# Performance work log

Measured on AMD Instinct MI355X. Metric: run time of the kernel, lower is better.

The kernel has to match this reference:

```python
import jax, jax.numpy as jnp
import numpy as np

# Module config (matches init_kwargs): inp_modes=[16,4,4,4], out_modes=[16,4,4,4], ranks=[1,8,8,1], 3x3 kernel
C_IN0, C_OUT0 = 16, 16          # leading conv channels
INP_MODES = (4, 4, 4)            # TT input modes -> c_inp = 64
OUT_MODES = (4, 4, 4)            # TT output modes -> c_out = 64
RANKS = (1, 8, 8, 1)
C_INP = int(np.prod(INP_MODES))  # 64
C_OUT = int(np.prod(OUT_MODES))  # 64


def setup_inputs() -> dict:
    key = jax.random.key(0)
    ks = jax.random.split(key, 5)
    x = jax.random.normal(ks[0], (8, C_IN0 * C_INP, 64, 64), jnp.float32)
    kernel = jax.random.normal(ks[1], (C_OUT0, C_IN0, 3, 3), jnp.float32) * (2.0 / (C_IN0 + C_OUT0))
    cores = {}
    for k in range(3):
        m, n = INP_MODES[k], OUT_MODES[k]
        cores[f"core{k}"] = jax.random.normal(ks[2 + k], (RANKS[k], m, n, RANKS[k + 1]), jnp.float32) * (2.0 / (m + n))
    b = jnp.ones((C_OUT,), jnp.float32)
    return {"x": x, "kernel": kernel, **cores, "b": b}


def _tt_matrix(core0, core1, core2):
    # Reconstruct W[(i1 i2 i3), (j1 j2 j3)] from TT cores (r_k, m_k, n_k, r_{k+1}).
    Wm = core0[0]  # (m1, n1, r1)  since r0 == 1
    for c in (core1, core2):
        Wm = jnp.einsum('...r,rmns->...mns', Wm, c)  # append (m_k, n_k) modes
    Wm = Wm[..., 0]  # drop trailing rank (== 1): (m1,n1,m2,n2,m3,n3)
    Wm = jnp.transpose(Wm, (0, 2, 4, 1, 3, 5))       # (m1,m2,m3,n1,n2,n3)
    return Wm.reshape(C_INP, C_OUT)


def reference(x, kernel, core0, core1, core2, b):
    B, Cin, H, W = x.shape  # Cin = C_IN0 * C_INP
    xr = x.reshape(-1, C_IN0, H, W)  # (B*c_inp, c_inp_0, H, W)
    y = jax.lax.conv_general_dilated(
        xr, kernel, window_strides=(1, 1), padding='VALID',
        dimension_numbers=('NCHW', 'OIHW', 'NCHW'))  # (B*c_inp, c_out_0, h, w)
    h, w = y.shape[-2], y.shape[-1]
    # Follow the torch reshape chain exactly
    y = y.reshape(B, C_INP, -1)                 # (B, c_inp, c_out_0*h*w)
    y = jnp.transpose(y, (0, 2, 1)).reshape(-1, C_INP)  # (B*c_out_0*h*w, c_inp)
    Wm = _tt_matrix(core0, core1, core2)        # (c_inp, c_out)
    out = y @ Wm + b                             # (B*c_out_0*h*w, c_out)
    return out.reshape(B, C_OUT0 * C_OUT, h, w)
```

## Files before the change

kernel.cpp:

```cpp
#include <hip/hip_runtime.h>
#include <hip/hip_bf16.h>

#define NB    8
#define NG    64
#define NCI   16
#define NC0   16
#define NJ    64
#define IH    64
#define IW    64
#define OH    62
#define OW    62
#define IPIX  4096
#define OPIX  3844

typedef __attribute__((ext_vector_type(8))) short  short8;
typedef __attribute__((ext_vector_type(4))) short  short4v;
typedef __attribute__((ext_vector_type(4))) float  float4v;

__device__ __forceinline__ unsigned short f2bf(float f) {
    unsigned int u = __builtin_bit_cast(unsigned int, f);
    unsigned int r = (u + 0x7fffu + ((u >> 16) & 1u)) >> 16;
    return (unsigned short)r;
}

__global__ __launch_bounds__(64) void prep_kernel(const float* __restrict__ K,
                                                  const float* __restrict__ c0_,
                                                  const float* __restrict__ c1_,
                                                  const float* __restrict__ c2_,
                                                  unsigned short* __restrict__ wmb,
                                                  unsigned short* __restrict__ kb) {
    int bi = blockIdx.x;
    int l  = threadIdx.x;
    if (bi < 8) {
        int jt = bi >> 1, kh = bi & 1;
        int j = jt * 16 + (l & 15);
        int j1 = j >> 4, j2 = (j >> 2) & 3, j3 = j & 3;
        for (int i = 0; i < 8; ++i) {
            int g = kh * 32 + (l >> 4) * 8 + i;
            int i1 = g >> 4, i2 = (g >> 2) & 3, i3 = g & 3;
            float s = 0.f;
            #pragma unroll
            for (int r1 = 0; r1 < 8; ++r1) {
                float a = c0_[(i1 * 4 + j1) * 8 + r1];
                float t = 0.f;
                #pragma unroll
                for (int r2 = 0; r2 < 8; ++r2) {
                    t += c1_[((r1 * 4 + i2) * 4 + j2) * 8 + r2] *
                         c2_[(r2 * 4 + i3) * 4 + j3];
                }
                s += a * t;
            }
            wmb[(bi * 64 + l) * 8 + i] = f2bf(s);
        }
    } else {
        int c0i = l & 15, q = l >> 4;
        for (int f = 0; f < 5; ++f) {
            int tap = f * 2 + (q >> 1);
            for (int i = 0; i < 8; ++i) {
                int ci = (q & 1) * 8 + i;
                float v = (tap < 9) ? K[(c0i * 16 + ci) * 9 + tap] : 0.f;
                kb[(f * 64 + l) * 8 + i] = f2bf(v);
            }
        }
    }
}

__global__ __launch_bounds__(256) void conv1_kernel(const float* __restrict__ x,
                                                    const unsigned short* __restrict__ kb,
                                                    unsigned short* __restrict__ y) {
    __shared__ unsigned short xl[18 * 16 * 68];
    int t    = threadIdx.x;
    int bi   = blockIdx.x;
    int band = bi & 3;
    int g    = (bi >> 2) & 63;
    int b    = bi >> 8;
    int y0   = band * 16;

    {
        int ci = t >> 4, part = t & 15;
        const float* xc = x + ((size_t)(b * 1024 + g * 16 + ci) * IPIX);
        #pragma unroll
        for (int s = 0; s < 18; ++s) {
            int row = y0 + s; if (row > 63) row = 63;
            float4v v = *(const float4v*)(xc + row * 64 + part * 4);
            unsigned short* dst = xl + (s * 16 + ci) * 68 + part * 4;
            dst[0] = f2bf(v[0]); dst[1] = f2bf(v[1]);
            dst[2] = f2bf(v[2]); dst[3] = f2bf(v[3]);
        }
    }
    for (int e = t; e < 576; e += 256) {
        int r = e >> 5, rem = e & 31;
        xl[(r * 16 + (rem >> 1)) * 68 + 64 + (rem & 1)] = 0;
    }
    __syncthreads();

    int lane = t & 63, wv = t >> 6;
    int ln = lane & 15, quad = lane >> 4;

    short8 kf[5];
    #pragma unroll
    for (int f = 0; f < 5; ++f)
        kf[f] = *(const short8*)(kb + (f * 64 + lane) * 8);

    int ci0 = (quad & 1) * 8;
    for (int k = 0; k < 16; ++k) {
        int tid = wv * 16 + k;
        int yr = tid >> 2, xt = tid & 3, x0 = xt * 16;
        int yo = y0 + yr;
        float4v acc = {0.f, 0.f, 0.f, 0.f};
        #pragma unroll
        for (int f = 0; f < 5; ++f) {
            int tap = f * 2 + (quad >> 1);
            if (tap > 8) tap = 8;
            int dy = tap / 3, dx = tap % 3;
            const unsigned short* base = xl + ((yr + dy) * 16 + ci0) * 68 + x0 + dx + ln;
            short8 a;
            #pragma unroll
            for (int i = 0; i < 8; ++i) a[i] = (short)base[i * 68];
            acc = __builtin_amdgcn_mfma_f32_16x16x32_bf16(a, kf[f], acc, 0, 0, 0);
        }
        if (yo < OH) {
            unsigned short* yp = y + ((size_t)(b * 1024 + g * 16 + ln) * 4096
                                      + yo * 64 + x0 + quad * 4);
            short4v o;
            o[0] = (short)f2bf(acc[0]); o[1] = (short)f2bf(acc[1]);
            o[2] = (short)f2bf(acc[2]); o[3] = (short)f2bf(acc[3]);
            *(short4v*)yp = o;
        }
    }
}

__global__ __launch_bounds__(512, 2) void mix3_kernel(const unsigned short* __restrict__ y,
                                                      const unsigned short* __restrict__ wmb,
                                                      const float* __restrict__ bias,
                                                      float* __restrict__ out) {
    __shared__ __align__(16) unsigned short yl[64 * 1024];
    int t    = threadIdx.x;
    int bi   = blockIdx.x;
    int prow = bi % OH;
    int b    = bi / OH;

    {
        int pq = t & 7, grp = t >> 3;
        const unsigned short* yb = y + ((size_t)b * 1024 * 4096) + prow * 64 + pq * 8;
        #pragma unroll
        for (int it = 0; it < 4; ++it) {
            int qd = it * 64 + grp;
            int gq = qd & 15, c0 = qd >> 4;
            const unsigned short* yp = yb + (size_t)(gq * 4 * 16 + c0) * 4096;
            short8 v0 = *(const short8*)(yp);
            short8 v1 = *(const short8*)(yp + 16 * 4096);
            short8 v2 = *(const short8*)(yp + 32 * 4096);
            short8 v3 = *(const short8*)(yp + 48 * 4096);
            int chunk = gq >> 1;
            int gof   = (gq & 1) * 4;
            #pragma unroll
            for (int pp = 0; pp < 8; ++pp) {
                int px = pq * 8 + pp;
                int csw = chunk ^ (c0 & 7) ^ (pq & 7);
                short4v u;
                u[0] = v0[pp]; u[1] = v1[pp]; u[2] = v2[pp]; u[3] = v3[pp];
                *(short4v*)(yl + px * 1024 + c0 * 64 + csw * 8 + gof) = u;
            }
        }
    }
    __syncthreads();

    int lane = t & 63, wv = t >> 6;
    int ln = lane & 15, quad = lane >> 4;

    short8 bf[8];
    #pragma unroll
    for (int q8 = 0; q8 < 8; ++q8)
        bf[q8] = *(const short8*)(wmb + (q8 * 64 + lane) * 8);

    float4v bv[4];
    #pragma unroll
    for (int jt = 0; jt < 4; ++jt)
        bv[jt] = *(const float4v*)(bias + jt * 16 + quad * 4);

    for (int kk = 0; kk < 8; ++kk) {
        int pl = wv * 8 + kk;
        const unsigned short* arow = yl + pl * 1024 + ln * 64;
        int sx = (ln & 7) ^ ((pl >> 3) & 7);
        short8 a0 = *(const short8*)(arow + (((0 + quad) ^ sx) * 8));
        short8 a1 = *(const short8*)(arow + (((4 + quad) ^ sx) * 8));
        if (pl < OW) {
            float* ob = out + (((size_t)(b * 16 + ln) * OPIX) + prow * OW + pl) * NJ
                        + quad * 4;
            #pragma unroll
            for (int jt = 0; jt < 4; ++jt) {
                float4v acc = bv[jt];
                acc = __builtin_amdgcn_mfma_f32_16x16x32_bf16(bf[jt * 2 + 0], a0, acc, 0, 0, 0);
                acc = __builtin_amdgcn_mfma_f32_16x16x32_bf16(bf[jt * 2 + 1], a1, acc, 0, 0, 0);
                *(float4v*)(ob + jt * 16) = acc;
            }
        }
    }
}

__global__ __launch_bounds__(64) void wm_kernel(const float* __restrict__ core0,
                                                const float* __restrict__ core1,
                                                const float* __restrict__ core2,
                                                float* __restrict__ Wm) {
    int g = threadIdx.x;
    int i1 = g >> 4, i2 = (g >> 2) & 3, i3 = g & 3;
    for (int j = 0; j < NJ; ++j) {
        int j1 = j >> 4, j2 = (j >> 2) & 3, j3 = j & 3;
        float s = 0.f;
        #pragma unroll
        for (int r1 = 0; r1 < 8; ++r1) {
            float a = core0[(i1 * 4 + j1) * 8 + r1];
            float t = 0.f;
            #pragma unroll
            for (int r2 = 0; r2 < 8; ++r2) {
                t += core1[((r1 * 4 + i2) * 4 + j2) * 8 + r2] *
                     core2[(r2 * 4 + i3) * 4 + j3];
            }
            s += a * t;
        }
        Wm[g * NJ + j] = s;
    }
}

__global__ __launch_bounds__(256) void fused_fallback(const float* __restrict__ x,
                                                      const float* __restrict__ K,
                                                      const float* __restrict__ Wm,
                                                      const float* __restrict__ bias,
                                                      float* __restrict__ out) {
    __shared__ float wlds[NG * NJ];
    __shared__ float klds[NCI * 9];
    int blk  = blockIdx.x;
    int pblk = blk & 15;
    int c0   = (blk >> 4) & 15;
    int b    = blk >> 8;
    for (int i = threadIdx.x; i < NG * NJ; i += 256) wlds[i] = Wm[i];
    for (int i = threadIdx.x; i < NCI * 9; i += 256) klds[i] = K[c0 * NCI * 9 + i];
    __syncthreads();

    int pix = pblk * 256 + threadIdx.x;
    if (pix >= OPIX) return;
    int yy = pix / OW;
    int xx = pix % OW;

    float acc[NJ];
    #pragma unroll
    for (int j = 0; j < NJ; ++j) acc[j] = 0.f;

    for (int g = 0; g < NG; ++g) {
        float c = 0.f;
        const float* xb = x + ((size_t)(b * NG + g) * NCI) * IPIX;
        for (int ci = 0; ci < NCI; ++ci) {
            #pragma unroll
            for (int dy = 0; dy < 3; ++dy) {
                #pragma unroll
                for (int dx = 0; dx < 3; ++dx) {
                    c += xb[ci * IPIX + (yy + dy) * IW + (xx + dx)] *
                         klds[ci * 9 + dy * 3 + dx];
                }
            }
        }
        const float4* wp = (const float4*)&wlds[g * NJ];
        #pragma unroll
        for (int j4 = 0; j4 < 16; ++j4) {
            float4 w = wp[j4];
            acc[j4 * 4 + 0] += w.x * c;
            acc[j4 * 4 + 1] += w.y * c;
            acc[j4 * 4 + 2] += w.z * c;
            acc[j4 * 4 + 3] += w.w * c;
        }
    }
    #pragma unroll
    for (int j = 0; j < NJ; ++j) {
        out[(((size_t)(b * NC0 + c0) * OPIX) + pix) * NJ + j] = acc[j] + bias[j];
    }
}

extern "C" void kernel_launch(void* const* d_in, const int* in_sizes, int n_in,
                              void* d_out, int out_size, void* d_ws, size_t ws_size,
                              hipStream_t stream) {
    const float* x     = (const float*)d_in[0];
    const float* K     = (const float*)d_in[1];
    const float* core0 = (const float*)d_in[2];
    const float* core1 = (const float*)d_in[3];
    const float* core2 = (const float*)d_in[4];
    const float* bias  = (const float*)d_in[5];
    float* out = (float*)d_out;

    const size_t z_off   = 16384;
    const size_t z_bytes = (size_t)NB * 1024 * 4096 * sizeof(unsigned short);

    if (ws_size >= z_off + z_bytes + 256) {
        unsigned short* wmb = (unsigned short*)d_ws;
        unsigned short* kb  = (unsigned short*)((char*)d_ws + 8192);
        unsigned short* y   = (unsigned short*)((char*)d_ws + z_off);
        prep_kernel<<<9, 64, 0, stream>>>(K, core0, core1, core2, wmb, kb);
        conv1_kernel<<<NB * NG * 4, 256, 0, stream>>>(x, kb, y);
        mix3_kernel<<<NB * OH, 512, 0, stream>>>(y, wmb, bias, out);
    } else {
        float* Wm = (float*)d_ws;
        wm_kernel<<<1, 64, 0, stream>>>(core0, core1, core2, Wm);
        fused_fallback<<<NB * NC0 * 16, 256, 0, stream>>>(x, K, Wm, bias, out);
    }
}
```

Before: 99.55 us.

## Store conv input tile channel-innermost in LDS for vectorized MFMA operand loads

Changes the shared-memory tile layout in conv1 from [row][ci][x] to [row][x][ci] with a padded pixel stride of 20. Each lane can then fetch its 8 channel values for an MFMA A-operand with two 8-byte LDS reads instead of eight scalar 2-byte reads. The global-to-LDS staging is reorganized so each thread loads four channels and writes packed short4 vectors. Per-tap offsets are also hoisted out of the inner loop. The risks are LDS bank conflicts from the new stride and a different global load pattern.

```diff
diff --git a/kernel.cpp b/kernel.cpp
--- a/kernel.cpp
+++ b/kernel.cpp
@@ -65,10 +65,13 @@
     }
 }
 
+#define PXS  20
+#define ROWS 1320
+
 __global__ __launch_bounds__(256) void conv1_kernel(const float* __restrict__ x,
                                                     const unsigned short* __restrict__ kb,
                                                     unsigned short* __restrict__ y) {
-    __shared__ unsigned short xl[18 * 16 * 68];
+    __shared__ unsigned short xl[18 * ROWS];
     int t    = threadIdx.x;
     int bi   = blockIdx.x;
     int band = bi & 3;
@@ -77,20 +80,32 @@
     int y0   = band * 16;
 
     {
-        int ci = t >> 4, part = t & 15;
-        const float* xc = x + ((size_t)(b * 1024 + g * 16 + ci) * IPIX);
-        #pragma unroll
-        for (int s = 0; s < 18; ++s) {
-            int row = y0 + s; if (row > 63) row = 63;
-            float4v v = *(const float4v*)(xc + row * 64 + part * 4);
-            unsigned short* dst = xl + (s * 16 + ci) * 68 + part * 4;
-            dst[0] = f2bf(v[0]); dst[1] = f2bf(v[1]);
-            dst[2] = f2bf(v[2]); dst[3] = f2bf(v[3]);
-        }
-    }
-    for (int e = t; e < 576; e += 256) {
-        int r = e >> 5, rem = e & 31;
-        xl[(r * 16 + (rem >> 1)) * 68 + 64 + (rem & 1)] = 0;
+        int part = t & 15, cig = (t >> 4) & 3, sg = t >> 6;
+        const float* xc = x + ((size_t)(b * 1024 + g * 16 + cig * 4) * IPIX) + part * 4;
+        #pragma unroll
+        for (int k = 0; k < 5; ++k) {
+            int s = sg + k * 4;
+            if (s < 18) {
+                int row = y0 + s; if (row > 63) row = 63;
+                const float* xr = xc + row * 64;
+                float4v v0 = *(const float4v*)(xr);
+                float4v v1 = *(const float4v*)(xr + IPIX);
+                float4v v2 = *(const float4v*)(xr + 2 * IPIX);
+                float4v v3 = *(const float4v*)(xr + 3 * IPIX);
+                unsigned short* dst = xl + s * ROWS + (part * 4) * PXS + cig * 4;
+                #pragma unroll
+                for (int p = 0; p < 4; ++p) {
+                    short4v u;
+                    u[0] = (short)f2bf(v0[p]); u[1] = (short)f2bf(v1[p]);
+                    u[2] = (short)f2bf(v2[p]); u[3] = (short)f2bf(v3[p]);
+                    *(short4v*)(dst + p * PXS) = u;
+                }
+            }
+        }
+    }
+    for (int e = t; e < 18 * 32; e += 256) {
+        int s = e >> 5, rem = e & 31;
+        xl[s * ROWS + (64 + (rem >> 4)) * PXS + (rem & 15)] = 0;
     }
     __syncthreads();
 
@@ -98,25 +113,29 @@
     int ln = lane & 15, quad = lane >> 4;
 
     short8 kf[5];
-    #pragma unroll
-    for (int f = 0; f < 5; ++f)
+    int off[5];
+    #pragma unroll
+    for (int f = 0; f < 5; ++f) {
         kf[f] = *(const short8*)(kb + (f * 64 + lane) * 8);
-
-    int ci0 = (quad & 1) * 8;
+        int tap = f * 2 + (quad >> 1);
+        if (tap > 8) tap = 8;
+        int dy = tap / 3, dx = tap % 3;
+        off[f] = dy * ROWS + dx * PXS;
+    }
+    int h8 = (quad & 1) * 8;
+
     for (int k = 0; k < 16; ++k) {
         int tid = wv * 16 + k;
-        int yr = tid >> 2, xt = tid & 3, x0 = xt * 16;
+        int yr = tid >> 2, x0 = (tid & 3) * 16;
         int yo = y0 + yr;
+        const unsigned short* base = xl + yr * ROWS + (x0 + ln) * PXS + h8;
         float4v acc = {0.f, 0.f, 0.f, 0.f};
         #pragma unroll
         for (int f = 0; f < 5; ++f) {
-            int tap = f * 2 + (quad >> 1);
-            if (tap > 8) tap = 8;
-            int dy = tap / 3, dx = tap % 3;
-            const unsigned short* base = xl + ((yr + dy) * 16 + ci0) * 68 + x0 + dx + ln;
-            short8 a;
-            #pragma unroll
-            for (int i = 0; i < 8; ++i) a[i] = (short)base[i * 68];
+            const unsigned short* p = base + off[f];
+            short4v lo = *(const short4v*)(p);
+            short4v hi = *(const short4v*)(p + 4);
+            short8 a = __builtin_shufflevector(lo, hi, 0, 1, 2, 3, 4, 5, 6, 7);
             acc = __builtin_amdgcn_mfma_f32_16x16x32_bf16(a, kf[f], acc, 0, 0, 0);
         }
         if (yo < OH) {
```

After: 99.10 us. About the same (-0.5%).
